# Kernel tuning notes

Hardware: AMD Instinct MI355X
Metric: run time of the kernel (lower is better)

The kernel has to match this reference:

```python
import jax, jax.numpy as jnp
import numpy as np

B, N, C, H, R = 16, 1024, 768, 12, 16
HD = C // H
SCALE = HD ** -0.5


def setup_inputs() -> dict:
    key = jax.random.key(0)
    ks = jax.random.split(key, 13)
    f = lambda k, shape, s=0.02: jax.random.normal(k, shape, dtype=jnp.float32) * s
    return {
        "x": jax.random.normal(ks[0], (B, N, C), dtype=jnp.float32),
        "W_qkv": f(ks[1], (3 * C, C)),
        "b_qkv": f(ks[2], (3 * C,)),
        "W_proj": f(ks[3], (C, C)),
        "b_proj": f(ks[4], (C,)),
        "A_q": f(ks[5], (R, C)),
        "B_q": f(ks[6], (C, R)),
        "A_k": f(ks[7], (R, C)),
        "B_k": f(ks[8], (C, R)),
        "A_v": f(ks[9], (R, C)),
        "B_v": f(ks[10], (C, R)),
        "A_o": f(ks[11], (R, C)),
        "B_o": f(ks[12], (C, R)),
    }


def _lora(x, A, Bu):
    # Adapter with no norm/act/bias, scaling=1.0: low-rank x @ A^T @ B^T
    return (x @ A.T) @ Bu.T


def _heads(t):
    # [B, N, C] -> [B, H, N, HD]
    return t.reshape(B, N, H, HD).transpose(0, 2, 1, 3)


def reference(x, W_qkv, b_qkv, W_proj, b_proj, A_q, B_q, A_k, B_k, A_v, B_v, A_o, B_o):
    qkv = x @ W_qkv.T + b_qkv                    # [B, N, 3C]
    qkv = qkv.reshape(B, N, 3, H, HD).transpose(2, 0, 3, 1, 4)  # [3, B, H, N, HD]
    q, k, v = qkv[0], qkv[1], qkv[2]
    q = q + _heads(_lora(x, A_q, B_q))
    k = k + _heads(_lora(x, A_k, B_k))
    v = v + _heads(_lora(x, A_v, B_v))
    attn = jnp.einsum("bhnd,bhmd->bhnm", q, k) * SCALE
    attn = jax.nn.softmax(attn, axis=-1)
    out = jnp.einsum("bhnm,bhmd->bhnd", attn, v)  # [B, H, N, HD]
    out = out.transpose(0, 2, 1, 3).reshape(B, N, C)
    out = out @ W_proj.T + b_proj
    out = out + _lora(out, A_o, B_o)
    return out
```

## Files before the change

### kernel.cpp

```cpp
#include <hip/hip_runtime.h>
#include <cmath>


#define DEVI __device__ __forceinline__

typedef float f32x4 __attribute__((ext_vector_type(4)));
typedef float f32x16 __attribute__((ext_vector_type(16)));
typedef short s16x8 __attribute__((ext_vector_type(8)));
typedef __bf16 b16x8 __attribute__((ext_vector_type(8)));
typedef unsigned int u32x4 __attribute__((ext_vector_type(4)));

static constexpr int MTOT = 16384;
static constexpr int C = 768;
static constexpr int N3 = 2304;

DEVI unsigned short f2bf(float x) {
  unsigned int u = __builtin_bit_cast(unsigned int, x);
  return (unsigned short)((u + 0x7FFFu + ((u >> 16) & 1u)) >> 16);
}

DEVI f32x4 mfma16(s16x8 a, s16x8 b, f32x4 c) {
  return __builtin_amdgcn_mfma_f32_16x16x32_bf16(
      __builtin_bit_cast(b16x8, a), __builtin_bit_cast(b16x8, b), c, 0, 0, 0);
}

DEVI f32x16 mfma32(s16x8 a, s16x8 b, f32x16 c) {
  return __builtin_amdgcn_mfma_f32_32x32x16_bf16(
      __builtin_bit_cast(b16x8, a), __builtin_bit_cast(b16x8, b), c, 0, 0, 0);
}

DEVI void async16(const void* g, void* l) {
  __builtin_amdgcn_global_load_lds(
      (__attribute__((address_space(1))) void*)g,
      (__attribute__((address_space(3))) void*)l, 16, 0, 0);
}

DEVI unsigned cvtpk_bf16(float lo, float hi2) {
  unsigned r;
  asm("v_cvt_pk_bf16_f32 %0, %1, %2" : "=v"(r) : "v"(lo), "v"(hi2));
  return r;
}


__global__ __launch_bounds__(256) void k_prep_x(const float* __restrict__ x,
                                                unsigned short* __restrict__ xb) {
  int idx = (blockIdx.x * 256 + threadIdx.x) * 4;
  float4 v = *(const float4*)(x + idx);
  uint2 p;
  p.x = (unsigned int)f2bf(v.x) | ((unsigned int)f2bf(v.y) << 16);
  p.y = (unsigned int)f2bf(v.z) | ((unsigned int)f2bf(v.w) << 16);
  *(uint2*)(xb + idx) = p;
}

__global__ __launch_bounds__(256) void k_prep_wqkv(
    const float* __restrict__ W, const float* __restrict__ Aq,
    const float* __restrict__ Bq, const float* __restrict__ Ak,
    const float* __restrict__ Bk, const float* __restrict__ Av,
    const float* __restrict__ Bv, unsigned short* __restrict__ out) {
  int idx = blockIdx.x * 256 + threadIdx.x;
  int n = idx / 768, c = idx - n * 768;
  int s = n / 768, co = n - s * 768;
  const float* A = (s == 0) ? Aq : (s == 1) ? Ak : Av;
  const float* Bm = (s == 0) ? Bq : (s == 1) ? Bk : Bv;
  float acc = W[idx];
#pragma unroll
  for (int r = 0; r < 16; ++r) acc += Bm[co * 16 + r] * A[r * 768 + c];
  out[idx] = f2bf(acc);
}

__global__ __launch_bounds__(256) void k_prep_M(const float* __restrict__ Ao,
                                                const float* __restrict__ Wp,
                                                float* __restrict__ M) {
  __shared__ float red[4][64];
  const int r = blockIdx.x, j0 = blockIdx.y * 64;
  const int jl = threadIdx.x & 63, cs = threadIdx.x >> 6;
  float acc = 0.f;
#pragma unroll 4
  for (int c = cs * 192; c < cs * 192 + 192; ++c)
    acc += Ao[r * 768 + c] * Wp[c * 768 + j0 + jl];
  red[cs][jl] = acc;
  __syncthreads();
  if (cs == 0)
    M[r * 768 + j0 + jl] = red[0][jl] + red[1][jl] + red[2][jl] + red[3][jl];
}

__global__ __launch_bounds__(256) void k_prep_wpe(const float* __restrict__ Wp,
                                                  const float* __restrict__ Bo,
                                                  const float* __restrict__ M,
                                                  unsigned short* __restrict__ out) {
  int idx = blockIdx.x * 256 + threadIdx.x;
  int n = idx / 768, j = idx - n * 768;
  float acc = Wp[idx];
#pragma unroll
  for (int r = 0; r < 16; ++r) acc += Bo[n * 16 + r] * M[r * 768 + j];
  out[idx] = f2bf(acc);
}

__global__ __launch_bounds__(256) void k_prep_beff(const float* __restrict__ bp,
                                                   const float* __restrict__ Ao,
                                                   const float* __restrict__ Bo,
                                                   float* __restrict__ beff) {
  __shared__ float red[256];
  __shared__ float bv[16];
  const int t = threadIdx.x;
  const int r = t >> 4, cs = t & 15;
  float a = 0.f;
#pragma unroll 4
  for (int c = cs * 48; c < cs * 48 + 48; ++c) a += Ao[r * 768 + c] * bp[c];
  red[t] = a;
  __syncthreads();
  if (cs == 0) {
    float s = 0.f;
#pragma unroll
    for (int k = 0; k < 16; ++k) s += red[r * 16 + k];
    bv[r] = s;
  }
  __syncthreads();
#pragma unroll
  for (int it = 0; it < 3; ++it) {
    const int n = it * 256 + t;
    float acc = bp[n];
#pragma unroll
    for (int r2 = 0; r2 < 16; ++r2) acc += Bo[n * 16 + r2] * bv[r2];
    beff[n] = acc;
  }
}


template <bool SWAP>
DEVI void qkv_body(const unsigned short* __restrict__ A,
                   const unsigned short* __restrict__ Bw,
                   const float* __restrict__ bias, int nblk,
                   unsigned short* __restrict__ qb,
                   unsigned short* __restrict__ kb,
                   unsigned short* __restrict__ vtb,
                   short (*la)[128 * 32], short (*lb)[128 * 32]) {
  const int t = threadIdx.x;
  const int w = t >> 6, l = t & 63;
  const int i = l & 15, qd = l >> 4;
  const int wm = w >> 1, wn = w & 1;
  const int mblk = blockIdx.x;

  const unsigned short* Ab = A + (size_t)(mblk * 128) * 768;
  const unsigned short* Bb = Bw + (size_t)(nblk * 128) * 768;
  const int sr = l >> 2;
  const int sc = (l & 3) * 8;

  auto stage = [&](int bufn, int kb_) {
    const int k0 = kb_ * 32;
#pragma unroll
    for (int j = 0; j < 2; ++j) {
      const int row = w * 32 + j * 16 + sr;
      async16(Ab + row * 768 + k0 + sc, &la[bufn][(w * 32 + j * 16) * 32]);
      async16(Bb + row * 768 + k0 + sc, &lb[bufn][(w * 32 + j * 16) * 32]);
    }
  };

  stage(0, 0);

  f32x4 acc[4][4] = {};

  for (int kb_ = 0; kb_ < 24; ++kb_) {
    const int buf = kb_ & 1;
    __syncthreads();
    if (kb_ < 23) stage(buf ^ 1, kb_ + 1);
    s16x8 af[4], bf[4];
#pragma unroll
    for (int mi = 0; mi < 4; ++mi)
      af[mi] = *(const s16x8*)&la[buf][(wm * 64 + mi * 16 + i) * 32 + qd * 8];
#pragma unroll
    for (int ni = 0; ni < 4; ++ni)
      bf[ni] = *(const s16x8*)&lb[buf][(wn * 64 + ni * 16 + i) * 32 + qd * 8];
#pragma unroll
    for (int mi = 0; mi < 4; ++mi)
#pragma unroll
      for (int ni = 0; ni < 4; ++ni) {
        if constexpr (SWAP)
          acc[mi][ni] = mfma16(bf[ni], af[mi], acc[mi][ni]);
        else
          acc[mi][ni] = mfma16(af[mi], bf[ni], acc[mi][ni]);
      }
  }

  const float c1 = 0.18033688011112042f;
  if constexpr (SWAP) {
#pragma unroll
    for (int ni = 0; ni < 4; ++ni) {
      const int n0 = nblk * 128 + wn * 64 + ni * 16 + qd * 4;
      const int s = n0 / 768;
      const int nrel = n0 - s * 768;
      const int h = nrel >> 6, d0 = nrel & 63;
      const float4 bv4 = *(const float4*)(bias + n0);
      unsigned short* dst = (s == 0) ? qb : kb;
      const float scl = (s == 0) ? c1 : 1.0f;
#pragma unroll
      for (int mi = 0; mi < 4; ++mi) {
        const int m = mblk * 128 + wm * 64 + mi * 16 + i;
        const int b = m >> 10, pos = m & 1023;
        uint2 pk;
        pk.x = (unsigned int)f2bf((acc[mi][ni][0] + bv4.x) * scl) |
               ((unsigned int)f2bf((acc[mi][ni][1] + bv4.y) * scl) << 16);
        pk.y = (unsigned int)f2bf((acc[mi][ni][2] + bv4.z) * scl) |
               ((unsigned int)f2bf((acc[mi][ni][3] + bv4.w) * scl) << 16);
        *(uint2*)&dst[(size_t)((b * 12 + h) * 1024 + pos) * 64 + d0] = pk;
      }
    }
  } else {
#pragma unroll
    for (int ni = 0; ni < 4; ++ni) {
      const int n = nblk * 128 + wn * 64 + ni * 16 + i;
      const int nrel = n - 1536;
      const int h = nrel >> 6, d = nrel & 63;
      const float bvv = bias[n];
#pragma unroll
      for (int mi = 0; mi < 4; ++mi) {
        const int m0 = mblk * 128 + wm * 64 + mi * 16 + qd * 4;
        const int b = m0 >> 10, pos0 = m0 & 1023;
        uint2 pk;
        pk.x = (unsigned int)f2bf(acc[mi][ni][0] + bvv) |
               ((unsigned int)f2bf(acc[mi][ni][1] + bvv) << 16);
        pk.y = (unsigned int)f2bf(acc[mi][ni][2] + bvv) |
               ((unsigned int)f2bf(acc[mi][ni][3] + bvv) << 16);
        *(uint2*)&vtb[(size_t)((b * 12 + h) * 64 + d) * 1024 + pos0] = pk;
      }
    }
  }
}

__global__ __launch_bounds__(256) void k_gemm_qkv(
    const unsigned short* __restrict__ A, const unsigned short* __restrict__ Bw,
    const float* __restrict__ bias, unsigned short* __restrict__ qb,
    unsigned short* __restrict__ kb, unsigned short* __restrict__ vtb) {
  __shared__ short la[2][128 * 32];
  __shared__ short lb[2][128 * 32];
  if (blockIdx.y < 12)
    qkv_body<true>(A, Bw, bias, blockIdx.y, qb, kb, vtb, la, lb);
  else
    qkv_body<false>(A, Bw, bias, blockIdx.y, qb, kb, vtb, la, lb);
}


__global__ __launch_bounds__(256, 2) void k_attn(
    const unsigned short* __restrict__ qg, const unsigned short* __restrict__ kg,
    const unsigned short* __restrict__ vtg, unsigned short* __restrict__ og) {
  __shared__ short k_lds[2][64 * 64];
  __shared__ short vt_lds[2][64 * 64];

  const int t = threadIdx.x;
  const int w = t >> 6, l = t & 63;
  const int lc = l & 31;
  const int hi = l >> 5;
  const int bh = blockIdx.x;
  const int qpair = blockIdx.y;
  const int h = bh % 12, b = bh / 12;

  const unsigned short* Qg = qg + (size_t)(bh * 1024 + qpair * 256) * 64;
  const unsigned short* Kg = kg + (size_t)bh * 1024 * 64;
  const unsigned short* Vtg = vtg + (size_t)bh * 64 * 1024;

  const int srl = l >> 3;
  const int sgc = (l & 7) ^ srl;

  s16x8 qfA[4], qfB[4];
#pragma unroll
  for (int kc = 0; kc < 4; ++kc) {
    qfA[kc] = *(const s16x8*)(Qg + (w * 32 + lc) * 64 + kc * 16 + hi * 8);
    qfB[kc] = *(const s16x8*)(Qg + (128 + w * 32 + lc) * 64 + kc * 16 + hi * 8);
  }

  int koffs[2][4];
#pragma unroll
  for (int pg = 0; pg < 2; ++pg)
#pragma unroll
    for (int kc = 0; kc < 4; ++kc)
      koffs[pg][kc] = (pg * 32 + lc) * 64 + (((kc * 2 + hi) ^ (lc & 7)) * 8);
  int voffs[2][4][2];
#pragma unroll
  for (int nd = 0; nd < 2; ++nd)
#pragma unroll
    for (int mi = 0; mi < 4; ++mi)
#pragma unroll
      for (int h2 = 0; h2 < 2; ++h2)
        voffs[nd][mi][h2] =
            (nd * 32 + lc) * 64 + (((2 * mi + h2) ^ (lc & 7)) * 8) + 4 * hi;

  auto stage = [&](int bufn, int tkv) {
#pragma unroll
    for (int it = 0; it < 2; ++it) {
      const int rbase = it * 32 + w * 8;
      async16(Kg + (size_t)(tkv * 64 + rbase + srl) * 64 + sgc * 8,
              &k_lds[bufn][rbase * 64]);
      async16(Vtg + (size_t)(rbase + srl) * 1024 + tkv * 64 + sgc * 8,
              &vt_lds[bufn][rbase * 64]);
    }
  };

  stage(0, 0);

  f32x16 oaccA[2] = {}, oaccB[2] = {};
  float llA = 0.f, llB = 0.f;

  for (int tkv = 0; tkv < 16; ++tkv) {
    const int buf = tkv & 1;
    __syncthreads();
    if (tkv < 15) stage(buf ^ 1, tkv + 1);

#pragma unroll
    for (int pg = 0; pg < 2; ++pg) {
      s16x8 ka[4];
#pragma unroll
      for (int kc = 0; kc < 4; ++kc)
        ka[kc] = *(const s16x8*)&k_lds[buf][koffs[pg][kc]];
      f32x16 stA = {}, stB = {};
#pragma unroll
      for (int kc = 0; kc < 4; ++kc) {
        stA = mfma32(ka[kc], qfA[kc], stA);
        stB = mfma32(ka[kc], qfB[kc], stB);
      }
      unsigned pkA[4][2], pkB[4][2];
#pragma unroll
      for (int q = 0; q < 4; ++q) {
        const float a0 = __builtin_amdgcn_exp2f(stA[4 * q + 0]);
        const float a1 = __builtin_amdgcn_exp2f(stA[4 * q + 1]);
        const float a2 = __builtin_amdgcn_exp2f(stA[4 * q + 2]);
        const float a3 = __builtin_amdgcn_exp2f(stA[4 * q + 3]);
        pkA[q][0] = cvtpk_bf16(a0, a1);
        pkA[q][1] = cvtpk_bf16(a2, a3);
        llA += (a0 + a1) + (a2 + a3);
        const float b0 = __builtin_amdgcn_exp2f(stB[4 * q + 0]);
        const float b1 = __builtin_amdgcn_exp2f(stB[4 * q + 1]);
        const float b2 = __builtin_amdgcn_exp2f(stB[4 * q + 2]);
        const float b3 = __builtin_amdgcn_exp2f(stB[4 * q + 3]);
        pkB[q][0] = cvtpk_bf16(b0, b1);
        pkB[q][1] = cvtpk_bf16(b2, b3);
        llB += (b0 + b1) + (b2 + b3);
      }
      __builtin_amdgcn_s_setprio(1);
#pragma unroll
      for (int m = 0; m < 2; ++m) {
        const int mi = pg * 2 + m;
        u32x4 faA, faB;
        faA[0] = pkA[2 * m][0];
        faA[1] = pkA[2 * m][1];
        faA[2] = pkA[2 * m + 1][0];
        faA[3] = pkA[2 * m + 1][1];
        faB[0] = pkB[2 * m][0];
        faB[1] = pkB[2 * m][1];
        faB[2] = pkB[2 * m + 1][0];
        faB[3] = pkB[2 * m + 1][1];
        const s16x8 pafA = __builtin_bit_cast(s16x8, faA);
        const s16x8 pafB = __builtin_bit_cast(s16x8, faB);
#pragma unroll
        for (int nd = 0; nd < 2; ++nd) {
          const uint2 vlo = *(const uint2*)&vt_lds[buf][voffs[nd][mi][0]];
          const uint2 vhi = *(const uint2*)&vt_lds[buf][voffs[nd][mi][1]];
          u32x4 vbu;
          vbu[0] = vlo.x;
          vbu[1] = vlo.y;
          vbu[2] = vhi.x;
          vbu[3] = vhi.y;
          const s16x8 vb = __builtin_bit_cast(s16x8, vbu);
          oaccA[nd] = mfma32(pafA, vb, oaccA[nd]);
          oaccB[nd] = mfma32(pafB, vb, oaccB[nd]);
        }
      }
      __builtin_amdgcn_s_setprio(0);
    }
  }

  const float lqA = llA + __shfl_xor(llA, 32, 64);
  const float lqB = llB + __shfl_xor(llB, 32, 64);
  float linvA[16], linvB[16];
#pragma unroll
  for (int r = 0; r < 16; ++r) {
    const int qr = (r & 3) + 8 * (r >> 2) + 4 * hi;
    linvA[r] = 1.0f / __shfl(lqA, qr, 64);
    linvB[r] = 1.0f / __shfl(lqB, qr, 64);
  }

  const int orow0 = qpair * 256 + w * 32;
#pragma unroll
  for (int nd = 0; nd < 2; ++nd)
#pragma unroll
    for (int r = 0; r < 16; ++r) {
      const int qr = (r & 3) + 8 * (r >> 2) + 4 * hi;
      const int d = nd * 32 + lc;
      og[(size_t)(b * 1024 + orow0 + qr) * 768 + h * 64 + d] =
          f2bf(oaccA[nd][r] * linvA[r]);
      og[(size_t)(b * 1024 + orow0 + 128 + qr) * 768 + h * 64 + d] =
          f2bf(oaccB[nd][r] * linvB[r]);
    }
}


__global__ __launch_bounds__(256) void k_gemm_proj(
    const unsigned short* __restrict__ A, const unsigned short* __restrict__ Bw,
    const float* __restrict__ bias, float* __restrict__ out) {
  __shared__ short la[2][128 * 32];
  __shared__ short lb[2][128 * 32];
  const int t = threadIdx.x;
  const int w = t >> 6, l = t & 63;
  const int i = l & 15, qd = l >> 4;
  const int wm = w >> 1, wn = w & 1;
  const int mblk = blockIdx.x, nblk = blockIdx.y;

  const unsigned short* Ab = A + (size_t)(mblk * 128) * 768;
  const unsigned short* Bb = Bw + (size_t)(nblk * 128) * 768;
  const int sr = l >> 2;
  const int sc = (l & 3) * 8;

  auto stage = [&](int bufn, int kb_) {
    const int k0 = kb_ * 32;
#pragma unroll
    for (int j = 0; j < 2; ++j) {
      const int row = w * 32 + j * 16 + sr;
      async16(Ab + row * 768 + k0 + sc, &la[bufn][(w * 32 + j * 16) * 32]);
      async16(Bb + row * 768 + k0 + sc, &lb[bufn][(w * 32 + j * 16) * 32]);
    }
  };

  stage(0, 0);

  f32x4 acc[4][4] = {};

  for (int kb_ = 0; kb_ < 24; ++kb_) {
    const int buf = kb_ & 1;
    __syncthreads();
    if (kb_ < 23) stage(buf ^ 1, kb_ + 1);
    s16x8 af[4], bf[4];
#pragma unroll
    for (int mi = 0; mi < 4; ++mi)
      af[mi] = *(const s16x8*)&la[buf][(wm * 64 + mi * 16 + i) * 32 + qd * 8];
#pragma unroll
    for (int ni = 0; ni < 4; ++ni)
      bf[ni] = *(const s16x8*)&lb[buf][(wn * 64 + ni * 16 + i) * 32 + qd * 8];
#pragma unroll
    for (int mi = 0; mi < 4; ++mi)
#pragma unroll
      for (int ni = 0; ni < 4; ++ni)
        acc[mi][ni] = mfma16(bf[ni], af[mi], acc[mi][ni]);
  }

#pragma unroll
  for (int ni = 0; ni < 4; ++ni) {
    const int n0 = nblk * 128 + wn * 64 + ni * 16 + qd * 4;
    const float4 bv4 = *(const float4*)(bias + n0);
#pragma unroll
    for (int mi = 0; mi < 4; ++mi) {
      const int m = mblk * 128 + wm * 64 + mi * 16 + i;
      float4 o;
      o.x = acc[mi][ni][0] + bv4.x;
      o.y = acc[mi][ni][1] + bv4.y;
      o.z = acc[mi][ni][2] + bv4.z;
      o.w = acc[mi][ni][3] + bv4.w;
      *(float4*)&out[(size_t)m * 768 + n0] = o;
    }
  }
}


extern "C" void kernel_launch(void* const* d_in, const int* in_sizes, int n_in,
                              void* d_out, int out_size, void* d_ws, size_t ws_size,
                              hipStream_t stream) {
  const float* x = (const float*)d_in[0];
  const float* Wqkv = (const float*)d_in[1];
  const float* bqkv = (const float*)d_in[2];
  const float* Wp = (const float*)d_in[3];
  const float* bp = (const float*)d_in[4];
  const float* Aq = (const float*)d_in[5];
  const float* Bq = (const float*)d_in[6];
  const float* Ak = (const float*)d_in[7];
  const float* Bk = (const float*)d_in[8];
  const float* Av = (const float*)d_in[9];
  const float* Bv = (const float*)d_in[10];
  const float* Ao = (const float*)d_in[11];
  const float* Bo = (const float*)d_in[12];
  float* out = (float*)d_out;

  unsigned short* xb = (unsigned short*)d_ws;
  unsigned short* wqkvb = xb + (size_t)MTOT * C;
  unsigned short* wpeb = wqkvb + (size_t)N3 * C;
  unsigned short* qb = wpeb + (size_t)C * C;
  unsigned short* kb = qb + (size_t)MTOT * C;
  unsigned short* vtb = kb + (size_t)MTOT * C;
  float* Mbuf = (float*)(vtb + (size_t)MTOT * C);
  float* beff = Mbuf + 16 * 768;
  unsigned short* ob = xb;

  k_prep_x<<<12288, 256, 0, stream>>>(x, xb);
  k_prep_wqkv<<<6912, 256, 0, stream>>>(Wqkv, Aq, Bq, Ak, Bk, Av, Bv, wqkvb);
  k_prep_M<<<dim3(16, 12), 256, 0, stream>>>(Ao, Wp, Mbuf);
  k_prep_wpe<<<2304, 256, 0, stream>>>(Wp, Bo, Mbuf, wpeb);
  k_prep_beff<<<1, 256, 0, stream>>>(bp, Ao, Bo, beff);

  k_gemm_qkv<<<dim3(128, 18), 256, 0, stream>>>(xb, wqkvb, bqkv, qb, kb, vtb);
  k_attn<<<dim3(192, 4), 256, 0, stream>>>(qb, kb, vtb, ob);
  k_gemm_proj<<<dim3(128, 6), 256, 0, stream>>>(ob, wpeb, beff, out);
}
```

Measured before the change: 350.3 us.

## Replace QKV and projection GEMMs with 256x256 swizzled pipelined 32x32 MFMA core

```diff
diff --git a/kernel.cpp b/kernel.cpp
--- a/kernel.cpp
+++ b/kernel.cpp
@@ -17,11 +17,6 @@
 DEVI unsigned short f2bf(float x) {
   unsigned int u = __builtin_bit_cast(unsigned int, x);
   return (unsigned short)((u + 0x7FFFu + ((u >> 16) & 1u)) >> 16);
-}
-
-DEVI f32x4 mfma16(s16x8 a, s16x8 b, f32x4 c) {
-  return __builtin_amdgcn_mfma_f32_16x16x32_bf16(
-      __builtin_bit_cast(b16x8, a), __builtin_bit_cast(b16x8, b), c, 0, 0, 0);
 }
 
 DEVI f32x16 mfma32(s16x8 a, s16x8 b, f32x16 c) {
@@ -128,115 +123,199 @@
 
 
 template <bool SWAP>
-DEVI void qkv_body(const unsigned short* __restrict__ A,
-                   const unsigned short* __restrict__ Bw,
-                   const float* __restrict__ bias, int nblk,
-                   unsigned short* __restrict__ qb,
-                   unsigned short* __restrict__ kb,
-                   unsigned short* __restrict__ vtb,
-                   short (*la)[128 * 32], short (*lb)[128 * 32]) {
+DEVI void g256_core(const unsigned short* __restrict__ Ag,
+                    const unsigned short* __restrict__ Bg,
+                    short* lds, f32x16 (&acc)[4][2]) {
   const int t = threadIdx.x;
   const int w = t >> 6, l = t & 63;
-  const int i = l & 15, qd = l >> 4;
-  const int wm = w >> 1, wn = w & 1;
-  const int mblk = blockIdx.x;
-
-  const unsigned short* Ab = A + (size_t)(mblk * 128) * 768;
-  const unsigned short* Bb = Bw + (size_t)(nblk * 128) * 768;
-  const int sr = l >> 2;
-  const int sc = (l & 3) * 8;
-
-  auto stage = [&](int bufn, int kb_) {
-    const int k0 = kb_ * 32;
-#pragma unroll
-    for (int j = 0; j < 2; ++j) {
-      const int row = w * 32 + j * 16 + sr;
-      async16(Ab + row * 768 + k0 + sc, &la[bufn][(w * 32 + j * 16) * 32]);
-      async16(Bb + row * 768 + k0 + sc, &lb[bufn][(w * 32 + j * 16) * 32]);
+  const int wm = w >> 2, wn = w & 3, lc = l & 31, hi = l >> 5;
+
+  int aoff[4][4], boff[2][4];
+#pragma unroll
+  for (int mi = 0; mi < 4; ++mi)
+#pragma unroll
+    for (int kc = 0; kc < 4; ++kc) {
+      const int rr = mi * 32 + lc;
+      aoff[mi][kc] = wm * 8192 + rr * 64 + (((kc * 2 + hi) ^ (rr & 7)) * 8);
+    }
+#pragma unroll
+  for (int nd = 0; nd < 2; ++nd)
+#pragma unroll
+    for (int kc = 0; kc < 4; ++kc) {
+      const int rr = (wn & 1) * 64 + nd * 32 + lc;
+      boff[nd][kc] =
+          16384 + (wn >> 1) * 8192 + rr * 64 + (((kc * 2 + hi) ^ (rr & 7)) * 8);
+    }
+
+  auto stageHT = [&](const unsigned short* G, int row0, int k0, int lbase) {
+#pragma unroll
+    for (int it = 0; it < 2; ++it) {
+      const int s16 = it * 512 + t;
+      const int rr = s16 >> 3;
+      const int cg = (s16 & 7) ^ (rr & 7);
+      async16(G + (size_t)(row0 + rr) * 768 + k0 + cg * 8, lds + lbase + s16 * 8);
     }
   };
 
-  stage(0, 0);
-
-  f32x4 acc[4][4] = {};
-
-  for (int kb_ = 0; kb_ < 24; ++kb_) {
-    const int buf = kb_ & 1;
-    __syncthreads();
-    if (kb_ < 23) stage(buf ^ 1, kb_ + 1);
-    s16x8 af[4], bf[4];
-#pragma unroll
-    for (int mi = 0; mi < 4; ++mi)
-      af[mi] = *(const s16x8*)&la[buf][(wm * 64 + mi * 16 + i) * 32 + qd * 8];
-#pragma unroll
-    for (int ni = 0; ni < 4; ++ni)
-      bf[ni] = *(const s16x8*)&lb[buf][(wn * 64 + ni * 16 + i) * 32 + qd * 8];
-#pragma unroll
-    for (int mi = 0; mi < 4; ++mi)
-#pragma unroll
-      for (int ni = 0; ni < 4; ++ni) {
-        if constexpr (SWAP)
-          acc[mi][ni] = mfma16(bf[ni], af[mi], acc[mi][ni]);
+  stageHT(Ag, 0, 0, 0);
+  stageHT(Ag, 128, 0, 8192);
+  stageHT(Bg, 0, 0, 16384);
+  stageHT(Bg, 128, 0, 24576);
+  stageHT(Bg, 0, 64, 32768 + 16384);
+  stageHT(Bg, 128, 64, 32768 + 24576);
+  asm volatile("s_waitcnt vmcnt(4)" ::: "memory");
+  asm volatile("s_barrier" ::: "memory");
+
+  for (int i = 0; i < 6; ++i) {
+    const int kY1 = (2 * i + 1) * 64;
+    const int kX2 = (2 * i + 2) * 64;
+    const int kY3 = (2 * i + 3) * 64;
+    const bool stX = (2 * i + 2) <= 11;
+    const bool stY = (2 * i + 3) <= 11;
+    s16x8 bf[2][4];
+#pragma unroll
+    for (int ph = 0; ph < 8; ++ph) {
+      const int tp = ph & 3;
+      const int cb = (ph < 4) ? 0 : 32768;
+      if (tp == 0) {
+#pragma unroll
+        for (int nd = 0; nd < 2; ++nd)
+#pragma unroll
+          for (int kc = 0; kc < 4; ++kc)
+            bf[nd][kc] = *(const s16x8*)&lds[cb + boff[nd][kc]];
+      }
+      s16x8 af[4];
+#pragma unroll
+      for (int kc = 0; kc < 4; ++kc)
+        af[kc] = *(const s16x8*)&lds[cb + aoff[tp][kc]];
+      if (ph == 0) stageHT(Ag, 0, kY1, 32768);
+      if (ph == 1) stageHT(Ag, 128, kY1, 32768 + 8192);
+      if (ph == 2 && stX) stageHT(Bg, 0, kX2, 16384);
+      if (ph == 3 && stX) stageHT(Bg, 128, kX2, 24576);
+      if (ph == 4 && stX) stageHT(Ag, 0, kX2, 0);
+      if (ph == 5 && stX) stageHT(Ag, 128, kX2, 8192);
+      if (ph == 6 && stY) stageHT(Bg, 0, kY3, 32768 + 16384);
+      if (ph == 7 && stY) stageHT(Bg, 128, kY3, 32768 + 24576);
+      asm volatile("s_barrier" ::: "memory");
+      __builtin_amdgcn_s_setprio(1);
+#pragma unroll
+      for (int kc = 0; kc < 4; ++kc)
+#pragma unroll
+        for (int nd = 0; nd < 2; ++nd) {
+          if constexpr (SWAP)
+            acc[tp][nd] = mfma32(bf[nd][kc], af[kc], acc[tp][nd]);
+          else
+            acc[tp][nd] = mfma32(af[kc], bf[nd][kc], acc[tp][nd]);
+        }
+      __builtin_amdgcn_s_setprio(0);
+      if (ph == 3) {
+        if (stX)
+          asm volatile("s_waitcnt vmcnt(4)" ::: "memory");
         else
-          acc[mi][ni] = mfma16(af[mi], bf[ni], acc[mi][ni]);
-      }
-  }
-
-  const float c1 = 0.18033688011112042f;
-  if constexpr (SWAP) {
-#pragma unroll
-    for (int ni = 0; ni < 4; ++ni) {
-      const int n0 = nblk * 128 + wn * 64 + ni * 16 + qd * 4;
-      const int s = n0 / 768;
-      const int nrel = n0 - s * 768;
-      const int h = nrel >> 6, d0 = nrel & 63;
-      const float4 bv4 = *(const float4*)(bias + n0);
-      unsigned short* dst = (s == 0) ? qb : kb;
-      const float scl = (s == 0) ? c1 : 1.0f;
-#pragma unroll
-      for (int mi = 0; mi < 4; ++mi) {
-        const int m = mblk * 128 + wm * 64 + mi * 16 + i;
-        const int b = m >> 10, pos = m & 1023;
-        uint2 pk;
-        pk.x = (unsigned int)f2bf((acc[mi][ni][0] + bv4.x) * scl) |
-               ((unsigned int)f2bf((acc[mi][ni][1] + bv4.y) * scl) << 16);
-        pk.y = (unsigned int)f2bf((acc[mi][ni][2] + bv4.z) * scl) |
-               ((unsigned int)f2bf((acc[mi][ni][3] + bv4.w) * scl) << 16);
-        *(uint2*)&dst[(size_t)((b * 12 + h) * 1024 + pos) * 64 + d0] = pk;
-      }
-    }
-  } else {
-#pragma unroll
-    for (int ni = 0; ni < 4; ++ni) {
-      const int n = nblk * 128 + wn * 64 + ni * 16 + i;
-      const int nrel = n - 1536;
-      const int h = nrel >> 6, d = nrel & 63;
-      const float bvv = bias[n];
-#pragma unroll
-      for (int mi = 0; mi < 4; ++mi) {
-        const int m0 = mblk * 128 + wm * 64 + mi * 16 + qd * 4;
-        const int b = m0 >> 10, pos0 = m0 & 1023;
-        uint2 pk;
-        pk.x = (unsigned int)f2bf(acc[mi][ni][0] + bvv) |
-               ((unsigned int)f2bf(acc[mi][ni][1] + bvv) << 16);
-        pk.y = (unsigned int)f2bf(acc[mi][ni][2] + bvv) |
-               ((unsigned int)f2bf(acc[mi][ni][3] + bvv) << 16);
-        *(uint2*)&vtb[(size_t)((b * 12 + h) * 64 + d) * 1024 + pos0] = pk;
-      }
-    }
-  }
-}
-
-__global__ __launch_bounds__(256) void k_gemm_qkv(
+          asm volatile("s_waitcnt vmcnt(0)" ::: "memory");
+      }
+      if (ph == 7)
+        asm volatile("s_waitcnt vmcnt(4)" ::: "memory");
+      asm volatile("s_barrier" ::: "memory");
+    }
+  }
+}
+
+
+__global__ __launch_bounds__(512, 2) void k_gemm_qkv256(
     const unsigned short* __restrict__ A, const unsigned short* __restrict__ Bw,
     const float* __restrict__ bias, unsigned short* __restrict__ qb,
     unsigned short* __restrict__ kb, unsigned short* __restrict__ vtb) {
-  __shared__ short la[2][128 * 32];
-  __shared__ short lb[2][128 * 32];
-  if (blockIdx.y < 12)
-    qkv_body<true>(A, Bw, bias, blockIdx.y, qb, kb, vtb, la, lb);
-  else
-    qkv_body<false>(A, Bw, bias, blockIdx.y, qb, kb, vtb, la, lb);
+  __shared__ short lds[65536];
+  const int t = threadIdx.x;
+  const int w = t >> 6, l = t & 63;
+  const int wm = w >> 2, wn = w & 3, lc = l & 31, hi = l >> 5;
+  const int mblk = blockIdx.x, nblk = blockIdx.y;
+  const unsigned short* Ag = A + (size_t)(mblk * 256) * 768;
+  const unsigned short* Bg = Bw + (size_t)(nblk * 256) * 768;
+  f32x16 acc[4][2] = {};
+  const int seg = nblk / 3;
+  const float c1 = 0.18033688011112042f;
+
+  if (seg < 2) {
+    g256_core<true>(Ag, Bg, lds, acc);
+    unsigned short* dst = (seg == 0) ? qb : kb;
+    const float scl = (seg == 0) ? c1 : 1.0f;
+#pragma unroll
+    for (int nd = 0; nd < 2; ++nd)
+#pragma unroll
+      for (int q2 = 0; q2 < 4; ++q2) {
+        const int n0 = nblk * 256 + wn * 64 + nd * 32 + q2 * 8 + 4 * hi;
+        const int nrel = n0 - seg * 768;
+        const int hh = nrel >> 6, d0 = nrel & 63;
+        const float4 bv4 = *(const float4*)(bias + n0);
+#pragma unroll
+        for (int mi = 0; mi < 4; ++mi) {
+          const int m = mblk * 256 + wm * 128 + mi * 32 + lc;
+          const int b = m >> 10, pos = m & 1023;
+          uint2 pk;
+          pk.x = (unsigned int)f2bf((acc[mi][nd][4 * q2 + 0] + bv4.x) * scl) |
+                 ((unsigned int)f2bf((acc[mi][nd][4 * q2 + 1] + bv4.y) * scl) << 16);
+          pk.y = (unsigned int)f2bf((acc[mi][nd][4 * q2 + 2] + bv4.z) * scl) |
+                 ((unsigned int)f2bf((acc[mi][nd][4 * q2 + 3] + bv4.w) * scl) << 16);
+          *(uint2*)&dst[(size_t)((b * 12 + hh) * 1024 + pos) * 64 + d0] = pk;
+        }
+      }
+  } else {
+    g256_core<false>(Ag, Bg, lds, acc);
+#pragma unroll
+    for (int nd = 0; nd < 2; ++nd) {
+      const int n = nblk * 256 + wn * 64 + nd * 32 + lc;
+      const int nrel = n - 1536;
+      const int hh = nrel >> 6, d = nrel & 63;
+      const float bvv = bias[n];
+#pragma unroll
+      for (int mi = 0; mi < 4; ++mi)
+#pragma unroll
+        for (int q2 = 0; q2 < 4; ++q2) {
+          const int m0 = mblk * 256 + wm * 128 + mi * 32 + q2 * 8 + 4 * hi;
+          const int b = m0 >> 10, pos0 = m0 & 1023;
+          uint2 pk;
+          pk.x = (unsigned int)f2bf(acc[mi][nd][4 * q2 + 0] + bvv) |
+                 ((unsigned int)f2bf(acc[mi][nd][4 * q2 + 1] + bvv) << 16);
+          pk.y = (unsigned int)f2bf(acc[mi][nd][4 * q2 + 2] + bvv) |
+                 ((unsigned int)f2bf(acc[mi][nd][4 * q2 + 3] + bvv) << 16);
+          *(uint2*)&vtb[(size_t)((b * 12 + hh) * 64 + d) * 1024 + pos0] = pk;
+        }
+    }
+  }
+}
+
+
+__global__ __launch_bounds__(512, 2) void k_gemm_proj256(
+    const unsigned short* __restrict__ A, const unsigned short* __restrict__ Bw,
+    const float* __restrict__ bias, float* __restrict__ out) {
+  __shared__ short lds[65536];
+  const int t = threadIdx.x;
+  const int w = t >> 6, l = t & 63;
+  const int wm = w >> 2, wn = w & 3, lc = l & 31, hi = l >> 5;
+  const int mblk = blockIdx.x, nblk = blockIdx.y;
+  const unsigned short* Ag = A + (size_t)(mblk * 256) * 768;
+  const unsigned short* Bg = Bw + (size_t)(nblk * 256) * 768;
+  f32x16 acc[4][2] = {};
+  g256_core<true>(Ag, Bg, lds, acc);
+#pragma unroll
+  for (int nd = 0; nd < 2; ++nd)
+#pragma unroll
+    for (int q2 = 0; q2 < 4; ++q2) {
+      const int n0 = nblk * 256 + wn * 64 + nd * 32 + q2 * 8 + 4 * hi;
+      const float4 bv4 = *(const float4*)(bias + n0);
+#pragma unroll
+      for (int mi = 0; mi < 4; ++mi) {
+        const int m = mblk * 256 + wm * 128 + mi * 32 + lc;
+        float4 o;
+        o.x = acc[mi][nd][4 * q2 + 0] + bv4.x;
+        o.y = acc[mi][nd][4 * q2 + 1] + bv4.y;
+        o.z = acc[mi][nd][4 * q2 + 2] + bv4.z;
+        o.w = acc[mi][nd][4 * q2 + 3] + bv4.w;
+        *(float4*)&out[(size_t)m * 768 + n0] = o;
+      }
+    }
 }
 
 
@@ -390,72 +469,6 @@
       og[(size_t)(b * 1024 + orow0 + 128 + qr) * 768 + h * 64 + d] =
           f2bf(oaccB[nd][r] * linvB[r]);
     }
-}
-
-
-__global__ __launch_bounds__(256) void k_gemm_proj(
-    const unsigned short* __restrict__ A, const unsigned short* __restrict__ Bw,
-    const float* __restrict__ bias, float* __restrict__ out) {
-  __shared__ short la[2][128 * 32];
-  __shared__ short lb[2][128 * 32];
-  const int t = threadIdx.x;
-  const int w = t >> 6, l = t & 63;
-  const int i = l & 15, qd = l >> 4;
-  const int wm = w >> 1, wn = w & 1;
-  const int mblk = blockIdx.x, nblk = blockIdx.y;
-
-  const unsigned short* Ab = A + (size_t)(mblk * 128) * 768;
-  const unsigned short* Bb = Bw + (size_t)(nblk * 128) * 768;
-  const int sr = l >> 2;
-  const int sc = (l & 3) * 8;
-
-  auto stage = [&](int bufn, int kb_) {
-    const int k0 = kb_ * 32;
-#pragma unroll
-    for (int j = 0; j < 2; ++j) {
-      const int row = w * 32 + j * 16 + sr;
-      async16(Ab + row * 768 + k0 + sc, &la[bufn][(w * 32 + j * 16) * 32]);
-      async16(Bb + row * 768 + k0 + sc, &lb[bufn][(w * 32 + j * 16) * 32]);
-    }
-  };
-
-  stage(0, 0);
-
-  f32x4 acc[4][4] = {};
-
-  for (int kb_ = 0; kb_ < 24; ++kb_) {
-    const int buf = kb_ & 1;
-    __syncthreads();
-    if (kb_ < 23) stage(buf ^ 1, kb_ + 1);
-    s16x8 af[4], bf[4];
-#pragma unroll
-    for (int mi = 0; mi < 4; ++mi)
-      af[mi] = *(const s16x8*)&la[buf][(wm * 64 + mi * 16 + i) * 32 + qd * 8];
-#pragma unroll
-    for (int ni = 0; ni < 4; ++ni)
-      bf[ni] = *(const s16x8*)&lb[buf][(wn * 64 + ni * 16 + i) * 32 + qd * 8];
-#pragma unroll
-    for (int mi = 0; mi < 4; ++mi)
-#pragma unroll
-      for (int ni = 0; ni < 4; ++ni)
-        acc[mi][ni] = mfma16(bf[ni], af[mi], acc[mi][ni]);
-  }
-
-#pragma unroll
-  for (int ni = 0; ni < 4; ++ni) {
-    const int n0 = nblk * 128 + wn * 64 + ni * 16 + qd * 4;
-    const float4 bv4 = *(const float4*)(bias + n0);
-#pragma unroll
-    for (int mi = 0; mi < 4; ++mi) {
-      const int m = mblk * 128 + wm * 64 + mi * 16 + i;
-      float4 o;
-      o.x = acc[mi][ni][0] + bv4.x;
-      o.y = acc[mi][ni][1] + bv4.y;
-      o.z = acc[mi][ni][2] + bv4.z;
-      o.w = acc[mi][ni][3] + bv4.w;
-      *(float4*)&out[(size_t)m * 768 + n0] = o;
-    }
-  }
 }
 
 
@@ -493,7 +506,7 @@
   k_prep_wpe<<<2304, 256, 0, stream>>>(Wp, Bo, Mbuf, wpeb);
   k_prep_beff<<<1, 256, 0, stream>>>(bp, Ao, Bo, beff);
 
-  k_gemm_qkv<<<dim3(128, 18), 256, 0, stream>>>(xb, wqkvb, bqkv, qb, kb, vtb);
+  k_gemm_qkv256<<<dim3(64, 9), 512, 0, stream>>>(xb, wqkvb, bqkv, qb, kb, vtb);
   k_attn<<<dim3(192, 4), 256, 0, stream>>>(qb, kb, vtb, ob);
-  k_gemm_proj<<<dim3(128, 6), 256, 0, stream>>>(ob, wpeb, beff, out);
-}
+  k_gemm_proj256<<<dim3(64, 3), 512, 0, stream>>>(ob, wpeb, beff, out);
+}
```

Result: slower. 364.0 us (+3.9%).
